# Kernel tuning notes

Hardware: AMD Instinct MI355X
Metric: run time of the kernel (lower is better)

The kernel has to match this reference:

```python
import jax, jax.numpy as jnp
import numpy as np

B, N, D, H, HID = 8, 512, 512, 8, 2048


def setup_inputs() -> dict:
    key = jax.random.key(0)
    ks = jax.random.split(key, 8)
    s = 0.02
    p = lambda i, shape: jax.random.normal(ks[i], shape, jnp.float32) * s
    return dict(
        x=jax.random.normal(ks[0], (B, N, D), jnp.float32),
        Wq=p(1, (D, D)), bq=jnp.zeros((D,), jnp.float32),
        Wk=p(2, (D, D)), bk=jnp.zeros((D,), jnp.float32),
        Wv=p(3, (D, D)), bv=jnp.zeros((D,), jnp.float32),
        Wsig=p(4, (H, D)), bsig=jnp.zeros((H,), jnp.float32),
        ln1_g=jnp.ones((D,), jnp.float32), ln1_b=jnp.zeros((D,), jnp.float32),
        W1=p(5, (HID, D)), b1=jnp.zeros((HID,), jnp.float32),
        W2=p(6, (D, HID)), b2=jnp.zeros((D,), jnp.float32),
        ln2_g=jnp.ones((D,), jnp.float32), ln2_b=jnp.zeros((D,), jnp.float32),
    )


def _ln(z, g, b, eps=1e-5):
    m = jnp.mean(z, axis=-1, keepdims=True)
    v = jnp.var(z, axis=-1, keepdims=True)
    return (z - m) * jax.lax.rsqrt(v + eps) * g + b


def reference(x, Wq, bq, Wk, bk, Wv, bv, Wsig, bsig,
              ln1_g, ln1_b, W1, b1, W2, b2, ln2_g, ln2_b):
    Bb, Nn, Dd = x.shape
    Hh = bsig.shape[0]
    dh = Dd // Hh
    # --- AnomalyAttention: series attention S, Gaussian prior P, Z = S @ V ---
    Q = (x @ Wq.T + bq).reshape(Bb, Nn, Hh, dh)
    K = (x @ Wk.T + bk).reshape(Bb, Nn, Hh, dh)
    V = (x @ Wv.T + bv).reshape(Bb, Nn, Hh, dh)
    scores = jnp.einsum('bnhd,bmhd->bhnm', Q, K) / jnp.sqrt(jnp.float32(dh))
    S = jax.nn.softmax(scores, axis=-1)                       # [B,H,N,N]
    # learned positive scale sigma per (batch, position, head)
    sigma = jax.nn.softplus(x @ Wsig.T + bsig) + 1e-5         # [B,N,H]
    idx = jnp.arange(Nn, dtype=jnp.float32)
    dist2 = (idx[:, None] - idx[None, :]) ** 2                # [N,N]
    sig = jnp.transpose(sigma, (0, 2, 1))[..., None]          # [B,H,N,1]
    gauss = jnp.exp(-dist2 / (2.0 * sig * sig)) / (jnp.sqrt(2.0 * jnp.pi) * sig)
    P = gauss / jnp.sum(gauss, axis=-1, keepdims=True)        # row-normalized prior
    Zh = jnp.einsum('bhnm,bmhd->bnhd', S, V).reshape(Bb, Nn, Dd)
    # --- residual + LayerNorm + MLP(relu) + residual + LayerNorm ---
    Z = _ln(Zh + x, ln1_g, ln1_b)
    hidden = jax.nn.relu(Z @ W1.T + b1)
    x_hat = hidden @ W2.T + b2
    x_hat = _ln(x_hat + Z, ln2_g, ln2_b)
    return (x_hat, P, S)
```

## Files before the change

### kernel.cpp

```cpp
#include <hip/hip_runtime.h>
#include <cstdint>

typedef short s16x8 __attribute__((ext_vector_type(8)));
typedef float f32x4 __attribute__((ext_vector_type(4)));
using u16 = unsigned short;


__device__ __forceinline__ u16 f2bf(float f) {
    union { float f; uint32_t u; } v; v.f = f;
    uint32_t u = v.u;
    return (u16)((u + 0x7FFFu + ((u >> 16) & 1u)) >> 16);
}
__device__ __forceinline__ float bf2f(u16 u) {
    return __uint_as_float(((uint32_t)u) << 16);
}

__device__ __forceinline__ void gload_lds16(const void* g, void* l) {
    __builtin_amdgcn_global_load_lds(
        (const __attribute__((address_space(1))) unsigned int*)g,
        (__attribute__((address_space(3))) unsigned int*)l, 16, 0, 0);
}

__device__ __forceinline__ void prior_row(
    const float* __restrict__ sigT, float* __restrict__ P, int row, int lane)
{
    int n = row & 511;
    float s = sigT[row];
    float a = -1.0f / (2.0f * s * s);
    float e[8]; float sum = 0.f;
#pragma unroll
    for (int j = 0; j < 8; ++j) {
        float d = (float)(n - (lane * 8 + j));
        e[j] = __expf(a * d * d);
        sum += e[j];
    }
#pragma unroll
    for (int m = 1; m < 64; m <<= 1) sum += __shfl_xor(sum, m, 64);
    float r = 1.0f / sum;
    f32x4* dst = (f32x4*)(P + (long)row * 512 + lane * 8);
    dst[0] = (f32x4){e[0]*r, e[1]*r, e[2]*r, e[3]*r};
    dst[1] = (f32x4){e[4]*r, e[5]*r, e[6]*r, e[7]*r};
}

__global__ __launch_bounds__(256) void k_convert_sigma(
    const float* __restrict__ x, const float* __restrict__ wq,
    const float* __restrict__ wk, const float* __restrict__ wv,
    const float* __restrict__ w1, const float* __restrict__ w2,
    const float* __restrict__ bq, const float* __restrict__ bk,
    const float* __restrict__ bv,
    const float* __restrict__ Wsig, const float* __restrict__ bsig,
    u16* __restrict__ xb, u16* __restrict__ wqb, u16* __restrict__ wkb,
    u16* __restrict__ wvb, u16* __restrict__ w1b, u16* __restrict__ w2b,
    float* __restrict__ biascat, float* __restrict__ sigT)
{
    int bk_ = blockIdx.x;
    int tid = threadIdx.x;
    if (bk_ >= 4866) {
        int row  = (int)(((bk_ - 4866) * 256 + tid) >> 6);
        int lane = tid & 63;
        const float4* xr = (const float4*)(x + (long)row * 512);
        float4 xa = xr[lane * 2], xc = xr[lane * 2 + 1];
        float xs[8] = {xa.x, xa.y, xa.z, xa.w, xc.x, xc.y, xc.z, xc.w};
        float ph[8];
#pragma unroll
        for (int h = 0; h < 8; ++h) {
            const float4* wr = (const float4*)(Wsig + h * 512);
            float4 wa = wr[lane * 2], wc = wr[lane * 2 + 1];
            ph[h] = xs[0]*wa.x + xs[1]*wa.y + xs[2]*wa.z + xs[3]*wa.w
                  + xs[4]*wc.x + xs[5]*wc.y + xs[6]*wc.z + xs[7]*wc.w;
        }
#pragma unroll
        for (int h = 0; h < 8; ++h)
#pragma unroll
            for (int m = 1; m < 64; m <<= 1)
                ph[h] += __shfl_xor(ph[h], m, 64);
        if (lane < 8) {
            float z  = ph[lane] + bsig[lane];
            float sp = fmaxf(z, 0.f) + log1pf(__expf(-fabsf(z)));
            int b = row >> 9, n = row & 511;
            sigT[(((long)b * 8 + lane) << 9) + n] = sp + 1e-5f;
        }
        return;
    }
    long g = (long)bk_ * 256 + tid;
    if (g >= 1245184) {
        long id = g - 1245184;
        if (id < 384) {
            const float* src = id < 128 ? bq : id < 256 ? bk : bv;
            ((float4*)biascat)[id] = ((const float4*)src)[id & 127];
        }
        return;
    }
    const float* src; u16* dst; long off;
    if      (g <  524288) { src = x;  dst = xb;  off = g; }
    else if (g <  589824) { src = wq; dst = wqb; off = g -  524288; }
    else if (g <  655360) { src = wk; dst = wkb; off = g -  589824; }
    else if (g <  720896) { src = wv; dst = wvb; off = g -  655360; }
    else if (g <  983040) { src = w1; dst = w1b; off = g -  720896; }
    else                  { src = w2; dst = w2b; off = g -  983040; }
    float4 v = ((const float4*)src)[off];
    ushort4 o;
    o.x = f2bf(v.x); o.y = f2bf(v.y); o.z = f2bf(v.z); o.w = f2bf(v.w);
    ((ushort4*)dst)[off] = o;
}

template<int EPI>
__device__ __forceinline__ void gemm_epi(
    const float* __restrict__ bias, void* __restrict__ C,
    int gi, int gj, float v)
{
    if constexpr (EPI == 3) {
        v = fmaxf(v + bias[gj], 0.f);
        ((u16*)C)[(long)gi * 2048 + gj] = f2bf(v);
    } else if constexpr (EPI == 4) {
        ((float*)C)[(long)gi * 512 + gj] = v + bias[gj];
    } else {
        v += bias[gj];
        int mat = gj >> 9, cj = gj & 511;
        int h = cj >> 6, d = cj & 63, b = gi >> 9, n = gi & 511;
        u16* base = (u16*)C;
        if (mat == 0)
            base[(((long)(b * 8 + h) * 512 + n) << 6) + d] = f2bf(v);
        else if (mat == 1)
            (base + 2097152)[(((long)(b * 8 + h) * 512 + n) << 6) + d] = f2bf(v);
        else
            (base + 4194304)[(((long)(b * 8 + h) * 64 + d) << 9) + n] = f2bf(v);
    }
}

template<int BM, int BN, int EPI>
__device__ __forceinline__ void gemm_body(
    const u16* __restrict__ A, const u16* __restrict__ B,
    const float* __restrict__ bias, void* __restrict__ C,
    int lda, int ldb, int K, int bx, int by,
    u16* __restrict__ As, u16* __restrict__ Bs)
{
    constexpr int BK = 64;
    const u16* Ag = A + (long)bx * BM * lda;
    const u16* Bg = B + (long)by * BN * ldb;

    int tid  = threadIdx.x;
    int wave = tid >> 6, lane = tid & 63;
    int wm = wave >> 2, wn = wave & 3;
    constexpr int WTM = BM / 2, WTN = BN / 4;
    constexpr int FM = WTM / 16, FN = WTN / 16;
    int r16 = lane & 15, g4 = lane >> 4;

    f32x4 acc[FM][FN];
#pragma unroll
    for (int i = 0; i < FM; ++i)
#pragma unroll
        for (int j = 0; j < FN; ++j) acc[i][j] = (f32x4){0.f, 0.f, 0.f, 0.f};

    constexpr int nA = BM * BK / (512 * 8);
    constexpr int nB = BN * BK / (512 * 8);

    auto stage = [&](int buf, int k0) {
#pragma unroll
        for (int c = 0; c < nA; ++c) {
            int e = c * 512 + tid;
            int r = e >> 3, s = e & 7;
            gload_lds16(Ag + (long)r * lda + k0 + ((s ^ (r & 7)) * 8),
                        &As[buf * BM * BK + e * 8]);
        }
#pragma unroll
        for (int c = 0; c < nB; ++c) {
            int e = c * 512 + tid;
            int r = e >> 3, s = e & 7;
            gload_lds16(Bg + (long)r * ldb + k0 + ((s ^ (r & 7)) * 8),
                        &Bs[buf * BN * BK + e * 8]);
        }
    };

    stage(0, 0);
    __syncthreads();
    int cur = 0;
    const int NT = K / BK;
    for (int t = 0; t < NT; ++t) {
        if (t + 1 < NT) stage(cur ^ 1, (t + 1) * BK);
#pragma unroll
        for (int kk = 0; kk < 2; ++kk) {
            s16x8 af[FM], bfr[FN];
#pragma unroll
            for (int fm = 0; fm < FM; ++fm) {
                int row = wm * WTM + fm * 16 + r16;
                int slot = (kk * 4 + g4) ^ (row & 7);
                af[fm] = *(const s16x8*)&As[cur * BM * BK + row * 64 + slot * 8];
            }
#pragma unroll
            for (int fn = 0; fn < FN; ++fn) {
                int row = wn * WTN + fn * 16 + r16;
                int slot = (kk * 4 + g4) ^ (row & 7);
                bfr[fn] = *(const s16x8*)&Bs[cur * BN * BK + row * 64 + slot * 8];
            }
#pragma unroll
            for (int fm = 0; fm < FM; ++fm)
#pragma unroll
                for (int fn = 0; fn < FN; ++fn)
                    acc[fm][fn] = __builtin_amdgcn_mfma_f32_16x16x32_bf16(af[fm], bfr[fn], acc[fm][fn], 0, 0, 0);
        }
        __syncthreads();
        cur ^= 1;
    }

    int i0 = bx * BM + wm * WTM;
    int j0 = by * BN + wn * WTN;
#pragma unroll
    for (int fm = 0; fm < FM; ++fm)
#pragma unroll
        for (int fn = 0; fn < FN; ++fn)
#pragma unroll
            for (int j = 0; j < 4; ++j)
                gemm_epi<EPI>(bias, C,
                              i0 + fm * 16 + (g4 << 2) + j,
                              j0 + fn * 16 + r16, acc[fm][fn][j]);
}

template<int BM, int BN, int EPI>
__global__ __launch_bounds__(512) void k_gemm_nt(
    const u16* __restrict__ A, const u16* __restrict__ B,
    const float* __restrict__ bias, void* __restrict__ C,
    int lda, int ldb, int K)
{
    __shared__ __align__(16) u16 As[2 * BM * 64];
    __shared__ __align__(16) u16 Bs[2 * BN * 64];
    gemm_body<BM, BN, EPI>(A, B, bias, C, lda, ldb, K,
                           blockIdx.x, blockIdx.y, As, Bs);
}

__global__ __launch_bounds__(512) void k_qkv_prior(
    const u16* __restrict__ A, const u16* __restrict__ B,
    const float* __restrict__ bias, void* __restrict__ C,
    const float* __restrict__ sigT, float* __restrict__ P)
{
    __shared__ __align__(16) u16 As[2 * 128 * 64];
    __shared__ __align__(16) u16 Bs[2 * 128 * 64];
    int gid = blockIdx.x;
    if (gid < 384) {
        gemm_body<128, 128, 5>(A, B, bias, C, 512, 512, 512,
                               gid % 32, gid / 32, As, Bs);
        return;
    }
    int pid  = gid - 384;
    int wave = threadIdx.x >> 6, lane = threadIdx.x & 63;
    prior_row(sigT, P, 16384 + pid * 8 + wave, lane);
}

__global__ __launch_bounds__(256, 4) void k_attn_prior(
    const u16* __restrict__ Qb, const u16* __restrict__ Kb,
    const u16* __restrict__ Vt, const float* __restrict__ sigT,
    float* __restrict__ S, float* __restrict__ Zh, float* __restrict__ P)
{
    __shared__ __align__(16) u16 Sb[4][16][264];
    __shared__ float cmbS[2][2][16];
    float* zc = (float*)&Sb[0][0][0];

    int gid = blockIdx.x;
    int tid = threadIdx.x;
    int wave = tid >> 6, lane = tid & 63;

    if (gid >= 1024) {
        prior_row(sigT, P, (gid - 1024) * 4 + wave, lane);
        return;
    }

    int bh = gid & 63;
    int rb = gid >> 6;
    int rg = wave >> 1, ch = wave & 1;
    int r16 = lane & 15, g4 = lane >> 4, hi8 = g4 * 8;

    int row0 = rb * 32 + rg * 16;
    const u16* Qg = Qb + ((long)bh * 512 + row0) * 64;
    const u16* Kg = Kb + ((long)bh * 512 + ch * 256) * 64;
    const u16* Vg = Vt + (long)bh * 64 * 512;

    s16x8 qa[2];
    qa[0] = *(const s16x8*)(Qg + r16 * 64 + hi8);
    qa[1] = *(const s16x8*)(Qg + r16 * 64 + 32 + hi8);

    float sm[4] = {0.f, 0.f, 0.f, 0.f};
    __builtin_amdgcn_s_setprio(1);
#pragma unroll
    for (int t = 0; t < 16; ++t) {
        f32x4 a = (f32x4){0.f, 0.f, 0.f, 0.f};
#pragma unroll
        for (int kk = 0; kk < 2; ++kk) {
            s16x8 b = *(const s16x8*)(Kg + (long)(t * 16 + r16) * 64 + kk * 32 + hi8);
            a = __builtin_amdgcn_mfma_f32_16x16x32_bf16(qa[kk], b, a, 0, 0, 0);
        }
#pragma unroll
        for (int j = 0; j < 4; ++j) {
            float p = __expf(0.125f * a[j]);
            sm[j] += p;
            Sb[wave][g4 * 4 + j][t * 16 + r16] = f2bf(p);
        }
    }
    __builtin_amdgcn_s_setprio(0);

#pragma unroll
    for (int j = 0; j < 4; ++j)
#pragma unroll
        for (int m = 1; m < 16; m <<= 1) sm[j] += __shfl_xor(sm[j], m, 64);
    if (r16 == 0) {
#pragma unroll
        for (int j = 0; j < 4; ++j) cmbS[rg][ch][g4 * 4 + j] = sm[j];
    }
    __syncthreads();

    float scale[4];
#pragma unroll
    for (int j = 0; j < 4; ++j)
        scale[j] = 1.0f / (cmbS[rg][0][g4 * 4 + j] + cmbS[rg][1][g4 * 4 + j]);

    long sbase = ((long)bh * 512 + row0) * 512 + ch * 256;
#pragma unroll
    for (int r = 0; r < 16; ++r) {
        float sc = 1.0f / (cmbS[rg][0][r] + cmbS[rg][1][r]);
        ushort4 u = *(const ushort4*)&Sb[wave][r][lane * 4];
        *(f32x4*)&S[sbase + (long)r * 512 + lane * 4] =
            (f32x4){bf2f(u.x) * sc, bf2f(u.y) * sc, bf2f(u.z) * sc, bf2f(u.w) * sc};
    }

    f32x4 zacc[4];
#pragma unroll
    for (int fn = 0; fn < 4; ++fn) zacc[fn] = (f32x4){0.f, 0.f, 0.f, 0.f};

    __builtin_amdgcn_s_setprio(1);
#pragma unroll
    for (int kb = 0; kb < 8; ++kb) {
        s16x8 pa = *(const s16x8*)&Sb[wave][r16][kb * 32 + hi8];
#pragma unroll
        for (int fn = 0; fn < 4; ++fn) {
            s16x8 vb = *(const s16x8*)(Vg + (long)(fn * 16 + r16) * 512 + ch * 256 + kb * 32 + hi8);
            zacc[fn] = __builtin_amdgcn_mfma_f32_16x16x32_bf16(pa, vb, zacc[fn], 0, 0, 0);
        }
    }
    __builtin_amdgcn_s_setprio(0);

    __syncthreads();
    if (ch == 1) {
#pragma unroll
        for (int fn = 0; fn < 4; ++fn)
#pragma unroll
            for (int j = 0; j < 4; ++j)
                zc[(rg * 16 + g4 * 4 + j) * 66 + fn * 16 + r16] = zacc[fn][j];
    }
    __syncthreads();
    if (ch == 0) {
        long zb = ((long)(bh >> 3) * 512 + row0) * 512 + (bh & 7) * 64;
#pragma unroll
        for (int fn = 0; fn < 4; ++fn)
#pragma unroll
            for (int j = 0; j < 4; ++j)
                Zh[zb + (long)(g4 * 4 + j) * 512 + fn * 16 + r16] =
                    (zacc[fn][j] + zc[(rg * 16 + g4 * 4 + j) * 66 + fn * 16 + r16])
                    * scale[j];
    }
}

template<bool WBF>
__global__ __launch_bounds__(256) void k_ln(
    const float* __restrict__ a, const float* __restrict__ b,
    const float* __restrict__ g, const float* __restrict__ bt,
    float* __restrict__ y, u16* __restrict__ yb)
{
    int row  = (int)((blockIdx.x * 256 + threadIdx.x) >> 6);
    int lane = threadIdx.x & 63;
    const float4* ar = (const float4*)(a + (long)row * 512);
    const float4* br = (const float4*)(b + (long)row * 512);
    float4 a0 = ar[lane * 2], a1 = ar[lane * 2 + 1];
    float4 b0 = br[lane * 2], b1 = br[lane * 2 + 1];
    float v[8] = {a0.x + b0.x, a0.y + b0.y, a0.z + b0.z, a0.w + b0.w,
                  a1.x + b1.x, a1.y + b1.y, a1.z + b1.z, a1.w + b1.w};
    float s = 0.f, q = 0.f;
#pragma unroll
    for (int j = 0; j < 8; ++j) { s += v[j]; q += v[j] * v[j]; }
#pragma unroll
    for (int m = 1; m < 64; m <<= 1) {
        s += __shfl_xor(s, m, 64);
        q += __shfl_xor(q, m, 64);
    }
    float mean = s * (1.f / 512.f);
    float var  = q * (1.f / 512.f) - mean * mean;
    float rstd = rsqrtf(var + 1e-5f);
    const float4* gr = (const float4*)(g + lane * 8);
    const float4* tr = (const float4*)(bt + lane * 8);
    float4 g0 = gr[0], g1 = gr[1], t0 = tr[0], t1 = tr[1];
    float gg[8] = {g0.x, g0.y, g0.z, g0.w, g1.x, g1.y, g1.z, g1.w};
    float tt[8] = {t0.x, t0.y, t0.z, t0.w, t1.x, t1.y, t1.z, t1.w};
    float o[8];
#pragma unroll
    for (int j = 0; j < 8; ++j) o[j] = (v[j] - mean) * rstd * gg[j] + tt[j];
    float4* yr = (float4*)(y + (long)row * 512 + lane * 8);
    yr[0] = make_float4(o[0], o[1], o[2], o[3]);
    yr[1] = make_float4(o[4], o[5], o[6], o[7]);
    if constexpr (WBF) {
        s16x8 ob;
#pragma unroll
        for (int j = 0; j < 8; ++j) ob[j] = (short)f2bf(o[j]);
        *(s16x8*)(yb + (long)row * 512 + lane * 8) = ob;
    }
}

extern "C" void kernel_launch(void* const* d_in, const int* in_sizes, int n_in,
                              void* d_out, int out_size, void* d_ws, size_t ws_size,
                              hipStream_t stream)
{
    const float* x    = (const float*)d_in[0];
    const float* Wq   = (const float*)d_in[1];
    const float* bq   = (const float*)d_in[2];
    const float* Wk   = (const float*)d_in[3];
    const float* bk   = (const float*)d_in[4];
    const float* Wv   = (const float*)d_in[5];
    const float* bv   = (const float*)d_in[6];
    const float* Wsig = (const float*)d_in[7];
    const float* bsig = (const float*)d_in[8];
    const float* g1   = (const float*)d_in[9];
    const float* be1  = (const float*)d_in[10];
    const float* W1   = (const float*)d_in[11];
    const float* b1   = (const float*)d_in[12];
    const float* W2   = (const float*)d_in[13];
    const float* b2   = (const float*)d_in[14];
    const float* g2   = (const float*)d_in[15];
    const float* be2  = (const float*)d_in[16];

    float* out_xhat = (float*)d_out;
    float* out_P    = out_xhat + 2097152;
    float* out_S    = out_P + 16777216;

    char* ws = (char*)d_ws;
    u16*   xb   = (u16*)(ws + 0);
    u16*   Qb   = (u16*)(ws + 4194304);
    u16*   hid  = (u16*)(ws + 0);
    u16*   Wqb  = (u16*)(ws + 16777216);
    u16*   W1b  = (u16*)(ws + 18350080);
    u16*   W2b  = (u16*)(ws + 20447232);
    float* sigT = (float*)(ws + 22544384);
    float* Zh   = (float*)(ws + 22675456);
    float* bcat = (float*)(ws + 22675456);
    float* x2   = (float*)(ws + 22675456);
    float* Z    = (float*)(ws + 31064064);
    u16*   Zb   = (u16*)(ws + 39452672);

    u16* Wkb = Wqb + 262144;
    u16* Wvb = Wqb + 524288;

    k_convert_sigma<<<5890, 256, 0, stream>>>(x, Wq, Wk, Wv, W1, W2, bq, bk, bv,
                                              Wsig, bsig,
                                              xb, Wqb, Wkb, Wvb, W1b, W2b,
                                              bcat, sigT);

    k_qkv_prior<<<2432, 512, 0, stream>>>(xb, Wqb, bcat, Qb, sigT, out_P);

    k_attn_prior<<<5120, 256, 0, stream>>>(Qb, Qb + 2097152, Qb + 4194304,
                                           sigT, out_S, Zh, out_P);

    k_ln<true><<<1024,256,0,stream>>>(Zh, x, g1, be1, Z, Zb);

    k_gemm_nt<128,128,3><<<dim3(32,16,1),512,0,stream>>>(Zb, W1b, b1, hid, 512, 512, 512);

    k_gemm_nt<64,128,4><<<dim3(64,4,1),512,0,stream>>>(hid, W2b, b2, x2, 2048, 2048, 2048);

    k_ln<false><<<1024,256,0,stream>>>(x2, Z, g2, be2, out_xhat, nullptr);
}
```

Before: 126.5 us.

## Redistribute Gaussian prior rows across QKV, attention and MLP GEMM kernels

The Gaussian prior P rows were previously computed as extra blocks in the QKV and attention kernels. This moves part of that work into the two MLP GEMM launches, which get tail blocks that each compute prior rows. The aim is to fill idle compute units in the small MLP GEMM grids and shorten the QKV and attention launches. The cost is a more complex partitioning of row ranges across four kernels, which must stay exactly consistent.

After: 128.5 us. Within noise of the previous version (+1.6%).

```diff
diff --git a/kernel.cpp b/kernel.cpp
--- a/kernel.cpp
+++ b/kernel.cpp
@@ -216,18 +216,6 @@
                               j0 + fn * 16 + r16, acc[fm][fn][j]);
 }
 
-template<int BM, int BN, int EPI>
-__global__ __launch_bounds__(512) void k_gemm_nt(
-    const u16* __restrict__ A, const u16* __restrict__ B,
-    const float* __restrict__ bias, void* __restrict__ C,
-    int lda, int ldb, int K)
-{
-    __shared__ __align__(16) u16 As[2 * BM * 64];
-    __shared__ __align__(16) u16 Bs[2 * BN * 64];
-    gemm_body<BM, BN, EPI>(A, B, bias, C, lda, ldb, K,
-                           blockIdx.x, blockIdx.y, As, Bs);
-}
-
 __global__ __launch_bounds__(512) void k_qkv_prior(
     const u16* __restrict__ A, const u16* __restrict__ B,
     const float* __restrict__ bias, void* __restrict__ C,
@@ -242,6 +230,42 @@
         return;
     }
     int pid  = gid - 384;
+    int wave = threadIdx.x >> 6, lane = threadIdx.x & 63;
+    prior_row(sigT, P, 22528 + pid * 8 + wave, lane);
+}
+
+__global__ __launch_bounds__(512) void k_mlp1_prior(
+    const u16* __restrict__ A, const u16* __restrict__ B,
+    const float* __restrict__ bias, void* __restrict__ C,
+    const float* __restrict__ sigT, float* __restrict__ P)
+{
+    __shared__ __align__(16) u16 As[2 * 128 * 64];
+    __shared__ __align__(16) u16 Bs[2 * 128 * 64];
+    int gid = blockIdx.x;
+    if (gid < 512) {
+        gemm_body<128, 128, 3>(A, B, bias, C, 512, 512, 512,
+                               gid & 31, gid >> 5, As, Bs);
+        return;
+    }
+    int pid  = gid - 512;
+    int wave = threadIdx.x >> 6, lane = threadIdx.x & 63;
+    prior_row(sigT, P, 8192 + pid * 8 + wave, lane);
+}
+
+__global__ __launch_bounds__(512) void k_mlp2_prior(
+    const u16* __restrict__ A, const u16* __restrict__ B,
+    const float* __restrict__ bias, void* __restrict__ C,
+    const float* __restrict__ sigT, float* __restrict__ P)
+{
+    __shared__ __align__(16) u16 As[2 * 64 * 64];
+    __shared__ __align__(16) u16 Bs[2 * 128 * 64];
+    int gid = blockIdx.x;
+    if (gid < 256) {
+        gemm_body<64, 128, 4>(A, B, bias, C, 2048, 2048, 2048,
+                              gid & 63, gid >> 6, As, Bs);
+        return;
+    }
+    int pid  = gid - 256;
     int wave = threadIdx.x >> 6, lane = threadIdx.x & 63;
     prior_row(sigT, P, 16384 + pid * 8 + wave, lane);
 }
@@ -450,16 +474,16 @@
                                               xb, Wqb, Wkb, Wvb, W1b, W2b,
                                               bcat, sigT);
 
-    k_qkv_prior<<<2432, 512, 0, stream>>>(xb, Wqb, bcat, Qb, sigT, out_P);
-
-    k_attn_prior<<<5120, 256, 0, stream>>>(Qb, Qb + 2097152, Qb + 4194304,
+    k_qkv_prior<<<1664, 512, 0, stream>>>(xb, Wqb, bcat, Qb, sigT, out_P);
+
+    k_attn_prior<<<3072, 256, 0, stream>>>(Qb, Qb + 2097152, Qb + 4194304,
                                            sigT, out_S, Zh, out_P);
 
     k_ln<true><<<1024,256,0,stream>>>(Zh, x, g1, be1, Z, Zb);
 
-    k_gemm_nt<128,128,3><<<dim3(32,16,1),512,0,stream>>>(Zb, W1b, b1, hid, 512, 512, 512);
-
-    k_gemm_nt<64,128,4><<<dim3(64,4,1),512,0,stream>>>(hid, W2b, b2, x2, 2048, 2048, 2048);
+    k_mlp1_prior<<<1536, 512, 0, stream>>>(Zb, W1b, b1, hid, sigT, out_P);
+
+    k_mlp2_prior<<<1024, 512, 0, stream>>>(hid, W2b, b2, x2, sigT, out_P);
 
     k_ln<false><<<1024,256,0,stream>>>(x2, Z, g2, be2, out_xhat, nullptr);
 }
```
